# Optimization experiments

Hardware: AMD Instinct MI355X
Metric: run time of the kernel (lower is better)

## Reference

```python
import jax, jax.numpy as jnp
import numpy as np

SEQ_LEN, BATCH, INPUT_SIZE, HIDDEN = 2048, 512, 1, 25


def setup_inputs() -> dict:
    key = jax.random.key(0)
    ks = jax.random.split(key, 7)
    s = 1.0 / np.sqrt(HIDDEN)  # PyTorch LSTM init scale (uniform(-s, s)); use scaled normal for simplicity
    return {
        "x": jax.random.normal(ks[0], (SEQ_LEN, BATCH, INPUT_SIZE), dtype=jnp.float32),
        "W_ih": jax.random.normal(ks[1], (4 * HIDDEN, INPUT_SIZE), dtype=jnp.float32) * s,
        "W_hh": jax.random.normal(ks[2], (4 * HIDDEN, HIDDEN), dtype=jnp.float32) * s,
        "b_ih": jax.random.normal(ks[3], (4 * HIDDEN,), dtype=jnp.float32) * s,
        "b_hh": jax.random.normal(ks[4], (4 * HIDDEN,), dtype=jnp.float32) * s,
        "W_lin": jax.random.normal(ks[5], (1, HIDDEN), dtype=jnp.float32) * s,
        "b_lin": jax.random.normal(ks[6], (1,), dtype=jnp.float32) * s,
    }


def reference(x, W_ih, W_hh, b_ih, b_hh, W_lin, b_lin):
    # x: [T, B, input_size]; PyTorch gate order: i, f, g, o
    T, B, _ = x.shape
    H = W_hh.shape[1]
    b = b_ih + b_hh  # [4H]

    def step(carry, xt):
        h, c = carry                                  # [B, H] each
        gates = xt @ W_ih.T + h @ W_hh.T + b          # [B, 4H]
        i, f, g, o = jnp.split(gates, 4, axis=-1)
        i = jax.nn.sigmoid(i)
        f = jax.nn.sigmoid(f)
        g = jnp.tanh(g)
        o = jax.nn.sigmoid(o)
        c_new = f * c + i * g
        h_new = o * jnp.tanh(c_new)
        return (h_new, c_new), h_new

    h0 = jnp.zeros((B, H), dtype=x.dtype)
    c0 = jnp.zeros((B, H), dtype=x.dtype)
    _, hs = jax.lax.scan(step, (h0, c0), x)           # hs: [T, B, H]
    pred = hs @ W_lin.T + b_lin                        # [T, B, output_size]
    return pred
```

## Files before the change

kernel.cpp:

```cpp
#include <hip/hip_runtime.h>

#define SEQ_LEN 2048
#define BATCH   512
#define HIDDEN  25

typedef int v2i __attribute__((ext_vector_type(2)));

__device__ __forceinline__ float fast_rcp(float v)  { return __builtin_amdgcn_rcpf(v); }
__device__ __forceinline__ float fast_exp2(float v) { return __builtin_amdgcn_exp2f(v); }

__device__ __forceinline__ float xswap32(float v) {
#if __has_builtin(__builtin_amdgcn_permlane32_swap)
    v2i r = __builtin_amdgcn_permlane32_swap(__float_as_int(v), __float_as_int(v), false, false);
    return (__int_as_float(r.x) + __int_as_float(r.y)) - v;
#else
    return __shfl_xor(v, 32);
#endif
}

__global__ __launch_bounds__(64)
__attribute__((amdgpu_waves_per_eu(1, 1)))
void lstm_kernel(
    const float* __restrict__ x,
    const float* __restrict__ W_ih,
    const float* __restrict__ W_hh,
    const float* __restrict__ b_ih,
    const float* __restrict__ b_hh,
    const float* __restrict__ W_lin,
    const float* __restrict__ b_lin,
    float* __restrict__ out)
{
    const int lane = threadIdx.x;
    const int b    = blockIdx.x;

    __shared__ float pp[64][29];

    const bool U  = (lane >= 32);
    const int  j  = lane & 31;
    const int  jj = (j < HIDDEN) ? j : 0;
    const bool hv = (j < HIDDEN);

    const int r1 = U ? (HIDDEN + jj) : jj;
    const int r2 = U ? (3 * HIDDEN + jj) : (2 * HIDDEN + jj);

    const float LOG2E = 1.4426950408889634f;
    const float s1 = -LOG2E;
    const float s2 = U ? -LOG2E : (-2.0f * LOG2E);

    float Wr1[HIDDEN], Wr2[HIDDEN];
    #pragma unroll
    for (int k = 0; k < HIDDEN; ++k) {
        Wr1[k] = W_hh[r1 * HIDDEN + k] * s1;
        Wr2[k] = W_hh[r2 * HIDDEN + k] * s2;
    }
    float bias1 = (b_ih[r1] + b_hh[r1]) * s1;
    float bias2 = (b_ih[r2] + b_hh[r2]) * s2;
    float wi1   = W_ih[r1] * s1;
    float wi2   = W_ih[r2] * s2;

    #pragma unroll
    for (int k = 0; k < HIDDEN; ++k) {
        asm volatile("" : "+v"(Wr1[k]));
        asm volatile("" : "+v"(Wr2[k]));
    }
    asm volatile("" : "+v"(bias1), "+v"(bias2), "+v"(wi1), "+v"(wi2));

    const float wlin  = (U && hv) ? W_lin[jj] : 0.0f;
    const float blin  = b_lin[0];
    const int   pcol  = (U && hv) ? jj : 26;

    float cs = 0.0f;
    float vh = 0.0f;

    const float* xb = x + b;
    float xv = xb[(size_t)lane * BATCH];

    #pragma unroll 1
    for (int tb = 0; tb < SEQ_LEN; tb += 64) {
        float xv_next = 0.0f;
        if (tb + 64 < SEQ_LEN) xv_next = xb[(size_t)(tb + 64 + lane) * BATCH];

        #pragma unroll 4
        for (int tt = 0; tt < 64; ++tt) {
            float hs[HIDDEN];
            #pragma unroll
            for (int k = 0; k < HIDDEN; ++k)
                hs[k] = __int_as_float(__builtin_amdgcn_readlane(__float_as_int(vh), 32 + k));

            const float xt = __int_as_float(__builtin_amdgcn_readlane(__float_as_int(xv), tt));

            float a1 = fmaf(xt, wi1, bias1);
            float a2 = fmaf(xt, wi2, bias2);
            float b1 = 0.0f, b2 = 0.0f;
            #pragma unroll
            for (int k = 0; k < 24; k += 2) {
                a1 = fmaf(hs[k],     Wr1[k],     a1);
                b1 = fmaf(hs[k + 1], Wr1[k + 1], b1);
                a2 = fmaf(hs[k],     Wr2[k],     a2);
                b2 = fmaf(hs[k + 1], Wr2[k + 1], b2);
            }
            a1 = fmaf(hs[24], Wr1[24], a1) + b1;
            a2 = fmaf(hs[24], Wr2[24], a2) + b2;

            const float R1 = fast_rcp(1.0f + fast_exp2(a1));
            const float R2 = fast_rcp(1.0f + fast_exp2(a2));

            const float Gp  = fmaf(R2, -4.0f * LOG2E, 2.0f * LOG2E);
            const float igs = R1 * Gp;
            const float igx = xswap32(igs);

            cs = fmaf(R1, cs, igx);
            const float R3 = fast_rcp(1.0f + fast_exp2(cs));
            const float o2 = R2 + R2;
            vh = fmaf(o2, R3, -R2);

            pp[tt][pcol] = vh * wlin;
        }
        __syncthreads();

        float s = blin;
        #pragma unroll
        for (int k = 0; k < HIDDEN; ++k) s += pp[lane][k];
        out[(size_t)(tb + lane) * BATCH + b] = s;
        __syncthreads();

        xv = xv_next;
    }
}

extern "C" void kernel_launch(void* const* d_in, const int* in_sizes, int n_in,
                              void* d_out, int out_size, void* d_ws, size_t ws_size,
                              hipStream_t stream) {
    const float* x     = (const float*)d_in[0];
    const float* W_ih  = (const float*)d_in[1];
    const float* W_hh  = (const float*)d_in[2];
    const float* b_ih  = (const float*)d_in[3];
    const float* b_hh  = (const float*)d_in[4];
    const float* W_lin = (const float*)d_in[5];
    const float* b_lin = (const float*)d_in[6];
    float* outp = (float*)d_out;

    hipLaunchKernelGGL(lstm_kernel, dim3(BATCH), dim3(64), 0, stream,
                       x, W_ih, W_hh, b_ih, b_hh, W_lin, b_lin, outp);
}
```

Before: 354.5 us.

## Pack recurrent weights and hidden state to fp16 and use dot2 instructions

Recurrent weights are converted to packed fp16 pairs, and each step the hidden state is packed with its DPP neighbour into fp16 pairs. This halves the per-step readlane broadcasts (13 instead of 25) and replaces 50 scalar FMAs with 26 v_dot2_f32_f16 ops on the serial critical path. The cost is fp16 rounding of weights and hidden state at every timestep, which may build up error over 2048 steps. A DPP swap and a pack conversion are added to each step.

```diff
diff --git a/kernel.cpp b/kernel.cpp
--- a/kernel.cpp
+++ b/kernel.cpp
@@ -5,9 +5,20 @@
 #define HIDDEN  25
 
 typedef int v2i __attribute__((ext_vector_type(2)));
+typedef _Float16 h2_t __attribute__((ext_vector_type(2)));
 
 __device__ __forceinline__ float fast_rcp(float v)  { return __builtin_amdgcn_rcpf(v); }
 __device__ __forceinline__ float fast_exp2(float v) { return __builtin_amdgcn_exp2f(v); }
+
+__device__ __forceinline__ float fdot2i(int a, int b, float c) {
+#if __has_builtin(__builtin_amdgcn_fdot2)
+    return __builtin_amdgcn_fdot2(__builtin_bit_cast(h2_t, a), __builtin_bit_cast(h2_t, b), c, false);
+#else
+    float d;
+    asm("v_dot2_f32_f16 %0, %1, %2, %3" : "=v"(d) : "v"(a), "v"(b), "v"(c));
+    return d;
+#endif
+}
 
 __device__ __forceinline__ float xswap32(float v) {
 #if __has_builtin(__builtin_amdgcn_permlane32_swap)
@@ -47,11 +58,18 @@
     const float s1 = -LOG2E;
     const float s2 = U ? -LOG2E : (-2.0f * LOG2E);
 
-    float Wr1[HIDDEN], Wr2[HIDDEN];
+    float w1[26], w2[26];
     #pragma unroll
     for (int k = 0; k < HIDDEN; ++k) {
-        Wr1[k] = W_hh[r1 * HIDDEN + k] * s1;
-        Wr2[k] = W_hh[r2 * HIDDEN + k] * s2;
+        w1[k] = W_hh[r1 * HIDDEN + k] * s1;
+        w2[k] = W_hh[r2 * HIDDEN + k] * s2;
+    }
+    w1[25] = 0.0f; w2[25] = 0.0f;
+    int W1p[13], W2p[13];
+    #pragma unroll
+    for (int m = 0; m < 13; ++m) {
+        W1p[m] = __builtin_bit_cast(int, __builtin_amdgcn_cvt_pkrtz(w1[2*m], w1[2*m+1]));
+        W2p[m] = __builtin_bit_cast(int, __builtin_amdgcn_cvt_pkrtz(w2[2*m], w2[2*m+1]));
     }
     float bias1 = (b_ih[r1] + b_hh[r1]) * s1;
     float bias2 = (b_ih[r2] + b_hh[r2]) * s2;
@@ -59,9 +77,9 @@
     float wi2   = W_ih[r2] * s2;
 
     #pragma unroll
-    for (int k = 0; k < HIDDEN; ++k) {
-        asm volatile("" : "+v"(Wr1[k]));
-        asm volatile("" : "+v"(Wr2[k]));
+    for (int m = 0; m < 13; ++m) {
+        asm volatile("" : "+v"(W1p[m]));
+        asm volatile("" : "+v"(W2p[m]));
     }
     asm volatile("" : "+v"(bias1), "+v"(bias2), "+v"(wi1), "+v"(wi2));
 
@@ -82,10 +100,14 @@
 
         #pragma unroll 4
         for (int tt = 0; tt < 64; ++tt) {
-            float hs[HIDDEN];
+            const int vhn = __builtin_amdgcn_mov_dpp(__float_as_int(vh), 0xB1, 0xF, 0xF, true);
+            const int hpk = __builtin_bit_cast(int,
+                __builtin_amdgcn_cvt_pkrtz(vh, __int_as_float(vhn)));
+
+            int hw[13];
             #pragma unroll
-            for (int k = 0; k < HIDDEN; ++k)
-                hs[k] = __int_as_float(__builtin_amdgcn_readlane(__float_as_int(vh), 32 + k));
+            for (int m = 0; m < 13; ++m)
+                hw[m] = __builtin_amdgcn_readlane(hpk, 32 + 2 * m);
 
             const float xt = __int_as_float(__builtin_amdgcn_readlane(__float_as_int(xv), tt));
 
@@ -93,14 +115,14 @@
             float a2 = fmaf(xt, wi2, bias2);
             float b1 = 0.0f, b2 = 0.0f;
             #pragma unroll
-            for (int k = 0; k < 24; k += 2) {
-                a1 = fmaf(hs[k],     Wr1[k],     a1);
-                b1 = fmaf(hs[k + 1], Wr1[k + 1], b1);
-                a2 = fmaf(hs[k],     Wr2[k],     a2);
-                b2 = fmaf(hs[k + 1], Wr2[k + 1], b2);
+            for (int m = 0; m < 12; m += 2) {
+                a1 = fdot2i(W1p[m],     hw[m],     a1);
+                b1 = fdot2i(W1p[m + 1], hw[m + 1], b1);
+                a2 = fdot2i(W2p[m],     hw[m],     a2);
+                b2 = fdot2i(W2p[m + 1], hw[m + 1], b2);
             }
-            a1 = fmaf(hs[24], Wr1[24], a1) + b1;
-            a2 = fmaf(hs[24], Wr2[24], a2) + b2;
+            a1 = fdot2i(W1p[12], hw[12], a1) + b1;
+            a2 = fdot2i(W2p[12], hw[12], a2) + b2;
 
             const float R1 = fast_rcp(1.0f + fast_exp2(a1));
             const float R2 = fast_rcp(1.0f + fast_exp2(a2));
```

Result: faster. 326.8 us (-7.8%).
